# Kernel optimization log

Measured on AMD Instinct MI355X. Metric: run time of the kernel, lower is better.

The kernel has to match this reference:

```python
import jax, jax.numpy as jnp
import numpy as np

EMBED_DIM = 768
NUM_HEADS = 12
HEAD_DIM = EMBED_DIM // NUM_HEADS
B, S = 2, 2048


def setup_inputs() -> dict:
    key = jax.random.key(0)
    ks = jax.random.split(key, 6)
    glorot = jnp.sqrt(6.0 / (EMBED_DIM + EMBED_DIM)).astype(jnp.float32)
    x = jax.random.normal(ks[0], (B, S, EMBED_DIM), dtype=jnp.float32)
    mask = jnp.zeros((1, 1, S, S), dtype=jnp.float32)  # additive mask, 0 = no masking
    Wq = jax.random.uniform(ks[1], (EMBED_DIM, EMBED_DIM), jnp.float32, -glorot, glorot)
    Wk = jax.random.uniform(ks[2], (EMBED_DIM, EMBED_DIM), jnp.float32, -glorot, glorot)
    Wv = jax.random.uniform(ks[3], (EMBED_DIM, EMBED_DIM), jnp.float32, -glorot, glorot)
    Wo = jax.random.uniform(ks[4], (EMBED_DIM, EMBED_DIM), jnp.float32, -glorot, glorot)
    bo = jnp.zeros((EMBED_DIM,), dtype=jnp.float32)
    return {"x": x, "mask": mask, "Wq": Wq, "Wk": Wk, "Wv": Wv, "Wo": Wo, "bo": bo}


def reference(x, mask, Wq, Wk, Wv, Wo, bo):
    b, s, _ = x.shape
    # Q/K/V projections (no bias), split into heads: [b, h, s, d]
    def split_heads(t):
        return t.reshape(b, s, NUM_HEADS, HEAD_DIM).transpose(0, 2, 1, 3)
    q = split_heads(x @ Wq)
    k = split_heads(x @ Wk)
    v = split_heads(x @ Wv)
    scale = 1.0 / jnp.sqrt(jnp.float32(HEAD_DIM))
    logits = jnp.einsum('bhqd,bhkd->bhqk', q, k) * scale  # [b, h, s, s]
    logits = logits + mask * (-1e9)
    weights = jax.nn.softmax(logits, axis=-1)
    attn = jnp.einsum('bhqk,bhkd->bhqd', weights, v)
    concat = attn.transpose(0, 2, 1, 3).reshape(b, s, EMBED_DIM)
    return concat @ Wo + bo
```

## Files before the change

kernel.cpp:

```cpp
#include <hip/hip_runtime.h>


typedef __bf16 bf16_t;
typedef bf16_t bf16x8 __attribute__((ext_vector_type(8)));
typedef bf16_t bf16x4 __attribute__((ext_vector_type(4)));
typedef float f32x4 __attribute__((ext_vector_type(4)));
typedef _Float16 f16x4 __attribute__((ext_vector_type(4)));

#define SC2 0.1803368801111137f

__device__ __forceinline__ float bf2f(unsigned short u) {
  union { unsigned int i; float f; } x;
  x.i = ((unsigned int)u) << 16;
  return x.f;
}

__device__ __forceinline__ void glds16(const bf16_t* g, bf16_t* l) {
  __builtin_amdgcn_global_load_lds(
      (const __attribute__((address_space(1))) void*)g,
      (__attribute__((address_space(3))) void*)l, 16, 0, 0);
}

__device__ __forceinline__ int detect_bf16_flag(const unsigned short* x) {
  const int lane = threadIdx.x & 63;
  const uint4* p = (const uint4*)x;
  uint4 a = p[lane * 2];
  uint4 b = p[lane * 2 + 1];
  unsigned int w[8] = {a.x, a.y, a.z, a.w, b.x, b.y, b.z, b.w};
  unsigned int big = 0;
#pragma unroll
  for (int i = 0; i < 8; i++) {
    unsigned int e0 = (w[i] >> 7) & 0xFF, e1 = (w[i] >> 23) & 0xFF;
    big |= (e0 > 0x88u) | (e1 > 0x88u);
  }
  unsigned long long bal = __ballot(big != 0u);
  return bal == 0ULL ? 1 : 0;
}

__global__ void k_prep(const void* __restrict__ x, const void* __restrict__ mask,
                       const void* __restrict__ Wq, const void* __restrict__ Wk,
                       const void* __restrict__ Wv, const void* __restrict__ Wo,
                       bf16_t* __restrict__ xb, bf16_t* __restrict__ wqkvT,
                       bf16_t* __restrict__ woT, int* __restrict__ mflags) {
  __shared__ float ts[32][33];
  __shared__ int snz;
  const int blk = blockIdx.x;
  const int f = detect_bf16_flag((const unsigned short*)x);

  if (blk < 1536) {
    int i = blk * 256 + threadIdx.x;
    if (f) {
      ((uint4*)xb)[i] = ((const uint4*)x)[i];
    } else {
      const float* xf = (const float*)x + (size_t)i * 8;
      bf16x8 v;
#pragma unroll
      for (int j = 0; j < 8; j++) v[j] = (bf16_t)xf[j];
      *(bf16x8*)(xb + (size_t)i * 8) = v;
    }
  } else if (blk < 3840) {
    const int t = blk - 1536;
    const int z = t / 576, r = t % 576, kt = r / 24, nt = r % 24;
    const void* wsrc = (z == 0) ? Wq : (z == 1) ? Wk : (z == 2) ? Wv : Wo;
    bf16_t* dst = (z < 3) ? (wqkvT + (size_t)z * 768 * 768) : woT;
    const int c = threadIdx.x & 31, r0 = threadIdx.x >> 5;
#pragma unroll
    for (int i = 0; i < 4; i++) {
      int kr = kt * 32 + r0 + i * 8;
      float v;
      if (f) v = bf2f(((const unsigned short*)wsrc)[(size_t)kr * 768 + nt * 32 + c]);
      else   v = ((const float*)wsrc)[(size_t)kr * 768 + nt * 32 + c];
      ts[r0 + i * 8][c] = v;
    }
    __syncthreads();
#pragma unroll
    for (int i = 0; i < 4; i++) {
      int nr = nt * 32 + r0 + i * 8;
      dst[(size_t)nr * 768 + kt * 32 + c] = (bf16_t)ts[c][r0 + i * 8];
    }
  } else {
    const int t = blk - 3840;
    const int qt = t >> 4, ktm = t & 15;
    if (threadIdx.x == 0) snz = 0;
    __syncthreads();
    int nz = 0;
    for (int i = 0; i < 64; i++) {
      int lin = i * 256 + threadIdx.x;
      int rr = lin >> 7, cc = lin & 127;
      size_t idx = (size_t)(qt * 128 + rr) * 2048 + ktm * 128 + cc;
      float v = f ? bf2f(((const unsigned short*)mask)[idx]) : ((const float*)mask)[idx];
      nz |= (v != 0.0f);
    }
    if (nz) snz = 1;
    __syncthreads();
    if (threadIdx.x == 0) mflags[qt * 16 + ktm] = snz;
  }
}

__global__ __launch_bounds__(256, 2) void k_gemmQKV(
    const bf16_t* __restrict__ A, const bf16_t* __restrict__ Bm,
    bf16_t* __restrict__ Qd, bf16_t* __restrict__ Kd, _Float16* __restrict__ Vt) {
  __shared__ __align__(16) char smem[17408];
  bf16_t* As = (bf16_t*)smem;
  bf16_t* Bs = (bf16_t*)(smem + 8192);
  _Float16* Tb = (_Float16*)smem;

  const int tid = threadIdx.x;
  const int n0 = blockIdx.x * 128, m0 = blockIdx.y * 128;
  const int r = tid >> 2, c8 = (tid & 3) << 3;
  const bf16_t* Ag = A + (size_t)(m0 + r) * 768 + c8;
  const bf16_t* Bg = Bm + (size_t)(n0 + r) * 768 + c8;
  const int wid = tid >> 6, lane = tid & 63;
  const int wm = (wid >> 1) << 6, wn = (wid & 1) << 6;
  const int lr = lane & 15, lk = (lane >> 4) << 3, g4 = (lane >> 4) << 2;

  f32x4 acc[4][4];
  const f32x4 z = {0.f, 0.f, 0.f, 0.f};
#pragma unroll
  for (int i = 0; i < 4; i++)
#pragma unroll
    for (int j = 0; j < 4; j++) acc[i][j] = z;

  for (int k0 = 0; k0 < 768; k0 += 32) {
    glds16(Ag + k0, As + wid * 512);
    glds16(Ag + (size_t)64 * 768 + k0, As + 2048 + wid * 512);
    glds16(Bg + k0, Bs + wid * 512);
    glds16(Bg + (size_t)64 * 768 + k0, Bs + 2048 + wid * 512);
    __syncthreads();
    bf16x8 af[4], bf_[4];
#pragma unroll
    for (int t = 0; t < 4; t++) af[t]  = *(const bf16x8*)&As[(wm + t * 16 + lr) * 32 + lk];
#pragma unroll
    for (int t = 0; t < 4; t++) bf_[t] = *(const bf16x8*)&Bs[(wn + t * 16 + lr) * 32 + lk];
#pragma unroll
    for (int i = 0; i < 4; i++)
#pragma unroll
      for (int j = 0; j < 4; j++)
        acc[i][j] = __builtin_amdgcn_mfma_f32_16x16x32_bf16(af[i], bf_[j], acc[i][j], 0, 0, 0);
    __syncthreads();
  }

  if (n0 < 1536) {
    bf16_t* dst = (n0 < 768) ? Qd : Kd;
    const int nb = (n0 < 768) ? n0 : n0 - 768;
    const int bb = m0 >> 11;
#pragma unroll
    for (int i = 0; i < 4; i++)
#pragma unroll
      for (int j = 0; j < 4; j++) {
        const int rc = nb + wn + j * 16 + lr;
        const int hh = rc >> 6, dd = rc & 63;
        const size_t base = (((size_t)bb * 12 + hh) * 2048) * 64 + dd;
#pragma unroll
        for (int reg = 0; reg < 4; reg++) {
          const int s = (m0 & 2047) + wm + i * 16 + g4 + reg;
          dst[base + (size_t)s * 64] = (bf16_t)acc[i][j][reg];
        }
      }
  } else {
    const int bb = m0 >> 11;
#pragma unroll
    for (int half = 0; half < 2; half++) {
      if ((wid & 1) == half) {
#pragma unroll
        for (int j = 0; j < 4; j++) {
          const int d_l = j * 16 + lr;
#pragma unroll
          for (int i = 0; i < 4; i++)
#pragma unroll
            for (int reg = 0; reg < 4; reg++)
              Tb[d_l * 136 + wm + i * 16 + g4 + reg] = (_Float16)acc[i][j][reg];
        }
      }
      __syncthreads();
      const int row = tid >> 2, cc = (tid & 3) * 32;
      const int vcol = (n0 - 1536) + half * 64 + row;
      const int hh = vcol >> 6;
      _Float16* dstv = Vt + (((size_t)bb * 12 + hh) * 64 + row) * 2048 + (m0 & 2047) + cc;
#pragma unroll
      for (int u = 0; u < 4; u++)
        *(uint4*)(dstv + u * 8) = *(const uint4*)&Tb[row * 136 + cc + u * 8];
      __syncthreads();
    }
  }
}

__global__ __launch_bounds__(320, 4) void k_flash(
    const bf16_t* __restrict__ Qd, const bf16_t* __restrict__ Kd,
    const _Float16* __restrict__ Vt, const void* __restrict__ mask,
    const int* __restrict__ mflags, const unsigned short* __restrict__ xdet,
    bf16_t* __restrict__ attn) {
  __shared__ __align__(16) char sm[32768];

  const int tid = threadIdx.x, wid = tid >> 6, lane = tid & 63;
  const int lr = lane & 15, quad = lane >> 4, lk = quad << 3, g4 = quad << 2;

  const int lin = blockIdx.x;
  const int gx = lin & 7, ww = lin >> 3;
  const int hb = gx * 3 + (ww >> 5);
  const int h = hb % 12, bb = hb / 12;
  const int qt = ww & 31;

  const size_t bh = (size_t)bb * 12 + h;
  const char* Kh = (const char*)(Kd + bh * 2048 * 64);
  const char* Vh = (const char*)(Vt + bh * 64 * 2048);

  if (wid == 4) {
    const char* kS[8]; const char* vS[8];
#pragma unroll
    for (int u = 0; u < 8; u++) {
      const int R = (u >> 1) * 16 + lr;
      const int c = (u & 1) * 4 + quad;
      kS[u] = Kh + R * 128 + c * 16;
      const int u2 = u * 2 + (lane >> 5);
      const int dtv = u2 & 3, ctv = u2 >> 2, j2 = lane & 31;
      vS[u] = Vh + (size_t)(dtv * 16 + (j2 & 15)) * 4096 + ctv * 32 + (j2 >> 4) * 16;
    }
    uint4 kv[8], vv[8];
#pragma unroll
    for (int u = 0; u < 8; u++) kv[u] = *(const uint4*)(kS[u]);
#pragma unroll
    for (int u = 0; u < 8; u++) vv[u] = *(const uint4*)(vS[u]);
#pragma unroll
    for (int u = 0; u < 8; u++) *(uint4*)(sm + u * 1024 + lane * 16) = kv[u];
#pragma unroll
    for (int u = 0; u < 8; u++) *(uint4*)(sm + 8192 + u * 1024 + lane * 16) = vv[u];
    __syncthreads();
    for (int s = 0; s < 32; s++) {
      if (s < 31) {
        const int t = s + 1;
        char* buf = sm + (t & 1) * 16384;
#pragma unroll
        for (int u = 0; u < 8; u++) kv[u] = *(const uint4*)(kS[u] + (size_t)t * 8192);
#pragma unroll
        for (int u = 0; u < 8; u++) vv[u] = *(const uint4*)(vS[u] + (size_t)t * 128);
#pragma unroll
        for (int u = 0; u < 8; u++) *(uint4*)(buf + u * 1024 + lane * 16) = kv[u];
#pragma unroll
        for (int u = 0; u < 8; u++) *(uint4*)(buf + 8192 + u * 1024 + lane * 16) = vv[u];
      }
      __syncthreads();
    }
    return;
  }

  const bf16_t* Qh = Qd + bh * 2048 * 64;
  const int q0 = qt * 64 + wid * 16;
  const int mbf = detect_bf16_flag(xdet);
  const int* mfrow = mflags + (qt >> 1) * 16;

  const bf16x8 qf0 = *(const bf16x8*)&Qh[(size_t)(q0 + lr) * 64 + lk];
  const bf16x8 qf1 = *(const bf16x8*)&Qh[(size_t)(q0 + lr) * 64 + 32 + lk];

  const f32x4 z = {0.f, 0.f, 0.f, 0.f};
  f32x4 ot[4];
#pragma unroll
  for (int dt = 0; dt < 4; dt++) ot[dt] = z;
  float mrow = -1e30f, lrow = 0.f;

  __syncthreads();

  for (int s = 0; s < 32; s++) {
    const char* Kc = sm + (s & 1) * 16384;
    const char* Vc = Kc + 8192;

    f32x4 sv[4];
#pragma unroll
    for (int ct = 0; ct < 4; ct++) sv[ct] = z;
#pragma unroll
    for (int ct = 0; ct < 4; ct++) {
      bf16x8 kf0 = *(const bf16x8*)(Kc + ct * 2048 + lane * 16);
      bf16x8 kf1 = *(const bf16x8*)(Kc + ct * 2048 + 1024 + lane * 16);
      sv[ct] = __builtin_amdgcn_mfma_f32_16x16x32_bf16(kf0, qf0, sv[ct], 0, 0, 0);
      sv[ct] = __builtin_amdgcn_mfma_f32_16x16x32_bf16(kf1, qf1, sv[ct], 0, 0, 0);
    }

    if (mfrow[s >> 1]) {
#pragma unroll
      for (int ct = 0; ct < 4; ct++)
#pragma unroll
        for (int reg = 0; reg < 4; reg++) {
          size_t mi = (size_t)(q0 + lr) * 2048 + s * 64 + ct * 16 + g4 + reg;
          float mv = mbf ? bf2f(((const unsigned short*)mask)[mi])
                         : ((const float*)mask)[mi];
          sv[ct][reg] -= 8e9f * mv;
        }
    }

    float t = fmaxf(
        fmaxf(fmaxf(fmaxf(sv[0][0], sv[0][1]), fmaxf(sv[0][2], sv[0][3])),
              fmaxf(fmaxf(sv[1][0], sv[1][1]), fmaxf(sv[1][2], sv[1][3]))),
        fmaxf(fmaxf(fmaxf(sv[2][0], sv[2][1]), fmaxf(sv[2][2], sv[2][3])),
              fmaxf(fmaxf(sv[3][0], sv[3][1]), fmaxf(sv[3][2], sv[3][3]))));
    t = fmaxf(t, __shfl_xor(t, 16));
    t = fmaxf(t, __shfl_xor(t, 32));
    const float mnew = fmaxf(mrow, t);
    const float alpha = exp2f((mrow - mnew) * SC2);
    const float mS = mnew * SC2;
    mrow = mnew;

    float rs = 0.f;
    f16x4 pb[4];
#pragma unroll
    for (int ct = 0; ct < 4; ct++) {
      float p0 = exp2f(fmaf(sv[ct][0], SC2, -mS));
      float p1 = exp2f(fmaf(sv[ct][1], SC2, -mS));
      float p2 = exp2f(fmaf(sv[ct][2], SC2, -mS));
      float p3 = exp2f(fmaf(sv[ct][3], SC2, -mS));
      rs += (p0 + p1) + (p2 + p3);
      f16x4 pk;
      pk[0] = (_Float16)p0; pk[1] = (_Float16)p1;
      pk[2] = (_Float16)p2; pk[3] = (_Float16)p3;
      pb[ct] = pk;
    }
    rs += __shfl_xor(rs, 16);
    rs += __shfl_xor(rs, 32);
    lrow = lrow * alpha + rs;

#pragma unroll
    for (int dt = 0; dt < 4; dt++)
#pragma unroll
      for (int reg = 0; reg < 4; reg++) ot[dt][reg] *= alpha;
#pragma unroll
    for (int ct = 0; ct < 4; ct++) {
#pragma unroll
      for (int dt = 0; dt < 4; dt++) {
        f16x4 va = *(const f16x4*)(Vc + (ct * 4 + dt) * 512 +
                                   (quad >> 1) * 256 + lr * 16 + (quad & 1) * 8);
        ot[dt] = __builtin_amdgcn_mfma_f32_16x16x16f16(va, pb[ct], ot[dt], 0, 0, 0);
      }
    }
    __syncthreads();
  }

  const float inv = 1.0f / lrow;
  bf16_t* arow = attn + ((size_t)bb * 2048 + q0 + lr) * 768 + h * 64 + g4;
#pragma unroll
  for (int dt = 0; dt < 4; dt++) {
    bf16x4 v;
#pragma unroll
    for (int reg = 0; reg < 4; reg++) v[reg] = (bf16_t)(ot[dt][reg] * inv);
    *(bf16x4*)(arow + dt * 16) = v;
  }
}

__global__ __launch_bounds__(256, 4) void k_gemm2(
    const bf16_t* __restrict__ A, const bf16_t* __restrict__ Bm,
    const void* __restrict__ bo, const unsigned short* __restrict__ xdet,
    float* __restrict__ outF, unsigned short* __restrict__ outH) {
  __shared__ __align__(16) bf16_t As[64 * 32];
  __shared__ __align__(16) bf16_t Bs[128 * 32];
  const int tid = threadIdx.x, wid = tid >> 6, lane = tid & 63;
  const int n0 = blockIdx.x * 128, m0 = blockIdx.y * 64;
  const int wm = (wid >> 1) * 32, wn = (wid & 1) * 64;
  const int lr = lane & 15, lk = (lane >> 4) << 3, g4 = (lane >> 4) << 2;
  const int rr = lane >> 2, c8 = (lane & 3) << 3;
  const bf16_t* Ag  = A + (size_t)(m0 + wid * 16 + rr) * 768 + c8;
  const bf16_t* Bg0 = Bm + (size_t)(n0 + wid * 32 + rr) * 768 + c8;
  const bf16_t* Bg1 = Bm + (size_t)(n0 + wid * 32 + 16 + rr) * 768 + c8;

  f32x4 acc[2][4];
  const f32x4 z = {0.f, 0.f, 0.f, 0.f};
#pragma unroll
  for (int i = 0; i < 2; i++)
#pragma unroll
    for (int j = 0; j < 4; j++) acc[i][j] = z;

  for (int k0 = 0; k0 < 768; k0 += 32) {
    glds16(Ag + k0, As + wid * 512);
    glds16(Bg0 + k0, Bs + wid * 1024);
    glds16(Bg1 + k0, Bs + wid * 1024 + 512);
    __syncthreads();
    bf16x8 af[2], bf_[4];
#pragma unroll
    for (int i = 0; i < 2; i++) af[i]  = *(const bf16x8*)&As[(wm + i * 16 + lr) * 32 + lk];
#pragma unroll
    for (int j = 0; j < 4; j++) bf_[j] = *(const bf16x8*)&Bs[(wn + j * 16 + lr) * 32 + lk];
#pragma unroll
    for (int i = 0; i < 2; i++)
#pragma unroll
      for (int j = 0; j < 4; j++)
        acc[i][j] = __builtin_amdgcn_mfma_f32_16x16x32_bf16(af[i], bf_[j], acc[i][j], 0, 0, 0);
    __syncthreads();
  }

  const int obf = detect_bf16_flag(xdet);
#pragma unroll
  for (int i = 0; i < 2; i++)
#pragma unroll
    for (int j = 0; j < 4; j++) {
      const int nn = n0 + wn + j * 16 + lr;
      const float bv = obf ? bf2f(((const unsigned short*)bo)[nn])
                           : ((const float*)bo)[nn];
#pragma unroll
      for (int reg = 0; reg < 4; reg++) {
        const int m = m0 + wm + i * 16 + g4 + reg;
        const float v = acc[i][j][reg] + bv;
        if (obf) outH[(size_t)m * 768 + nn] = __builtin_bit_cast(unsigned short, (bf16_t)v);
        else     outF[(size_t)m * 768 + nn] = v;
      }
    }
}

extern "C" void kernel_launch(void* const* d_in, const int* in_sizes, int n_in,
                              void* d_out, int out_size, void* d_ws, size_t ws_size,
                              hipStream_t stream) {
  (void)in_sizes; (void)n_in; (void)out_size; (void)ws_size;
  const void* x    = d_in[0];
  const void* mask = d_in[1];
  const void* Wq   = d_in[2];
  const void* Wk   = d_in[3];
  const void* Wv   = d_in[4];
  const void* Wo   = d_in[5];
  const void* bo   = d_in[6];

  char* w = (char*)d_ws;
  size_t off = 0;
  auto take = [&](size_t b) -> void* {
    void* p = w + off;
    off = (off + b + 255) & ~(size_t)255;
    return p;
  };
  int*      mflags = (int*)take(256 * 4);
  bf16_t*   wqkvT  = (bf16_t*)take((size_t)2304 * 768 * 2);
  bf16_t*   woT    = (bf16_t*)take((size_t)768 * 768 * 2);
  bf16_t*   xb     = (bf16_t*)take((size_t)4096 * 768 * 2);
  bf16_t*   Qd     = (bf16_t*)take((size_t)3145728 * 2);
  bf16_t*   Kd     = (bf16_t*)take((size_t)3145728 * 2);
  _Float16* Vt     = (_Float16*)take((size_t)3145728 * 2);
  bf16_t*   attn   = xb;

  k_prep<<<4096, 256, 0, stream>>>(x, mask, Wq, Wk, Wv, Wo, xb, wqkvT, woT, mflags);
  k_gemmQKV<<<dim3(18, 32), 256, 0, stream>>>(xb, wqkvT, Qd, Kd, Vt);
  k_flash<<<768, 320, 0, stream>>>(Qd, Kd, Vt, mask, mflags,
                                   (const unsigned short*)x, attn);
  k_gemm2<<<dim3(6, 64), 256, 0, stream>>>(attn, woT, bo, (const unsigned short*)x,
                                           (float*)d_out, (unsigned short*)d_out);
}
```

Measured before the change: 201.5 us.

## Process two query tiles per flash wave with fewer waves and lazy rescale

Each compute wave in the flash kernel now handles 32 query rows (two 16-row groups) instead of 16. The block shrinks to two compute waves plus one loader wave, so each K/V fragment read from LDS feeds twice as many MFMAs. The mask-tile flags are preloaded into a bitmask, and the output/denominator rescale is skipped when no row maximum grows. The QKV GEMM launch-bounds occupancy hint rises from 2 to 3. This raises register pressure per wave and halves the wave count per block, which could reduce latency hiding.

```diff
diff --git a/kernel.cpp b/kernel.cpp
--- a/kernel.cpp
+++ b/kernel.cpp
@@ -97,7 +97,7 @@
   }
 }
 
-__global__ __launch_bounds__(256, 2) void k_gemmQKV(
+__global__ __launch_bounds__(256, 3) void k_gemmQKV(
     const bf16_t* __restrict__ A, const bf16_t* __restrict__ Bm,
     bf16_t* __restrict__ Qd, bf16_t* __restrict__ Kd, _Float16* __restrict__ Vt) {
   __shared__ __align__(16) char smem[17408];
@@ -185,7 +185,7 @@
   }
 }
 
-__global__ __launch_bounds__(320, 4) void k_flash(
+__global__ __launch_bounds__(192, 4) void k_flash(
     const bf16_t* __restrict__ Qd, const bf16_t* __restrict__ Kd,
     const _Float16* __restrict__ Vt, const void* __restrict__ mask,
     const int* __restrict__ mflags, const unsigned short* __restrict__ xdet,
@@ -205,7 +205,7 @@
   const char* Kh = (const char*)(Kd + bh * 2048 * 64);
   const char* Vh = (const char*)(Vt + bh * 64 * 2048);
 
-  if (wid == 4) {
+  if (wid == 2) {
     const char* kS[8]; const char* vS[8];
 #pragma unroll
     for (int u = 0; u < 8; u++) {
@@ -245,18 +245,27 @@
   }
 
   const bf16_t* Qh = Qd + bh * 2048 * 64;
-  const int q0 = qt * 64 + wid * 16;
+  const int q0 = qt * 64 + wid * 32;
   const int mbf = detect_bf16_flag(xdet);
   const int* mfrow = mflags + (qt >> 1) * 16;
-
-  const bf16x8 qf0 = *(const bf16x8*)&Qh[(size_t)(q0 + lr) * 64 + lk];
-  const bf16x8 qf1 = *(const bf16x8*)&Qh[(size_t)(q0 + lr) * 64 + 32 + lk];
+  int mbits = 0;
+#pragma unroll
+  for (int t = 0; t < 16; t++) mbits |= (mfrow[t] != 0) << t;
+
+  bf16x8 qf[2][2];
+#pragma unroll
+  for (int qg = 0; qg < 2; qg++) {
+    qf[qg][0] = *(const bf16x8*)&Qh[(size_t)(q0 + qg * 16 + lr) * 64 + lk];
+    qf[qg][1] = *(const bf16x8*)&Qh[(size_t)(q0 + qg * 16 + lr) * 64 + 32 + lk];
+  }
 
   const f32x4 z = {0.f, 0.f, 0.f, 0.f};
-  f32x4 ot[4];
-#pragma unroll
-  for (int dt = 0; dt < 4; dt++) ot[dt] = z;
-  float mrow = -1e30f, lrow = 0.f;
+  f32x4 ot[2][4];
+  float mrow[2] = {-1e30f, -1e30f}, lrow[2] = {0.f, 0.f};
+#pragma unroll
+  for (int qg = 0; qg < 2; qg++)
+#pragma unroll
+    for (int dt = 0; dt < 4; dt++) ot[qg][dt] = z;
 
   __syncthreads();
 
@@ -264,83 +273,106 @@
     const char* Kc = sm + (s & 1) * 16384;
     const char* Vc = Kc + 8192;
 
-    f32x4 sv[4];
-#pragma unroll
-    for (int ct = 0; ct < 4; ct++) sv[ct] = z;
+    f32x4 sv[2][4];
+#pragma unroll
+    for (int qg = 0; qg < 2; qg++)
+#pragma unroll
+      for (int ct = 0; ct < 4; ct++) sv[qg][ct] = z;
 #pragma unroll
     for (int ct = 0; ct < 4; ct++) {
       bf16x8 kf0 = *(const bf16x8*)(Kc + ct * 2048 + lane * 16);
       bf16x8 kf1 = *(const bf16x8*)(Kc + ct * 2048 + 1024 + lane * 16);
-      sv[ct] = __builtin_amdgcn_mfma_f32_16x16x32_bf16(kf0, qf0, sv[ct], 0, 0, 0);
-      sv[ct] = __builtin_amdgcn_mfma_f32_16x16x32_bf16(kf1, qf1, sv[ct], 0, 0, 0);
-    }
-
-    if (mfrow[s >> 1]) {
-#pragma unroll
-      for (int ct = 0; ct < 4; ct++)
-#pragma unroll
-        for (int reg = 0; reg < 4; reg++) {
-          size_t mi = (size_t)(q0 + lr) * 2048 + s * 64 + ct * 16 + g4 + reg;
-          float mv = mbf ? bf2f(((const unsigned short*)mask)[mi])
-                         : ((const float*)mask)[mi];
-          sv[ct][reg] -= 8e9f * mv;
-        }
-    }
-
-    float t = fmaxf(
-        fmaxf(fmaxf(fmaxf(sv[0][0], sv[0][1]), fmaxf(sv[0][2], sv[0][3])),
-              fmaxf(fmaxf(sv[1][0], sv[1][1]), fmaxf(sv[1][2], sv[1][3]))),
-        fmaxf(fmaxf(fmaxf(sv[2][0], sv[2][1]), fmaxf(sv[2][2], sv[2][3])),
-              fmaxf(fmaxf(sv[3][0], sv[3][1]), fmaxf(sv[3][2], sv[3][3]))));
-    t = fmaxf(t, __shfl_xor(t, 16));
-    t = fmaxf(t, __shfl_xor(t, 32));
-    const float mnew = fmaxf(mrow, t);
-    const float alpha = exp2f((mrow - mnew) * SC2);
-    const float mS = mnew * SC2;
-    mrow = mnew;
-
-    float rs = 0.f;
-    f16x4 pb[4];
-#pragma unroll
-    for (int ct = 0; ct < 4; ct++) {
-      float p0 = exp2f(fmaf(sv[ct][0], SC2, -mS));
-      float p1 = exp2f(fmaf(sv[ct][1], SC2, -mS));
-      float p2 = exp2f(fmaf(sv[ct][2], SC2, -mS));
-      float p3 = exp2f(fmaf(sv[ct][3], SC2, -mS));
-      rs += (p0 + p1) + (p2 + p3);
-      f16x4 pk;
-      pk[0] = (_Float16)p0; pk[1] = (_Float16)p1;
-      pk[2] = (_Float16)p2; pk[3] = (_Float16)p3;
-      pb[ct] = pk;
-    }
-    rs += __shfl_xor(rs, 16);
-    rs += __shfl_xor(rs, 32);
-    lrow = lrow * alpha + rs;
-
-#pragma unroll
-    for (int dt = 0; dt < 4; dt++)
-#pragma unroll
-      for (int reg = 0; reg < 4; reg++) ot[dt][reg] *= alpha;
+      sv[0][ct] = __builtin_amdgcn_mfma_f32_16x16x32_bf16(kf0, qf[0][0], sv[0][ct], 0, 0, 0);
+      sv[0][ct] = __builtin_amdgcn_mfma_f32_16x16x32_bf16(kf1, qf[0][1], sv[0][ct], 0, 0, 0);
+      sv[1][ct] = __builtin_amdgcn_mfma_f32_16x16x32_bf16(kf0, qf[1][0], sv[1][ct], 0, 0, 0);
+      sv[1][ct] = __builtin_amdgcn_mfma_f32_16x16x32_bf16(kf1, qf[1][1], sv[1][ct], 0, 0, 0);
+    }
+
+    if ((mbits >> (s >> 1)) & 1) {
+#pragma unroll
+      for (int qg = 0; qg < 2; qg++)
+#pragma unroll
+        for (int ct = 0; ct < 4; ct++)
+#pragma unroll
+          for (int reg = 0; reg < 4; reg++) {
+            size_t mi = (size_t)(q0 + qg * 16 + lr) * 2048 + s * 64 + ct * 16 + g4 + reg;
+            float mv = mbf ? bf2f(((const unsigned short*)mask)[mi])
+                           : ((const float*)mask)[mi];
+            sv[qg][ct][reg] -= 8e9f * mv;
+          }
+    }
+
+    float mnew[2];
+#pragma unroll
+    for (int qg = 0; qg < 2; qg++) {
+      float t = fmaxf(
+          fmaxf(fmaxf(fmaxf(sv[qg][0][0], sv[qg][0][1]), fmaxf(sv[qg][0][2], sv[qg][0][3])),
+                fmaxf(fmaxf(sv[qg][1][0], sv[qg][1][1]), fmaxf(sv[qg][1][2], sv[qg][1][3]))),
+          fmaxf(fmaxf(fmaxf(sv[qg][2][0], sv[qg][2][1]), fmaxf(sv[qg][2][2], sv[qg][2][3])),
+                fmaxf(fmaxf(sv[qg][3][0], sv[qg][3][1]), fmaxf(sv[qg][3][2], sv[qg][3][3]))));
+      t = fmaxf(t, __shfl_xor(t, 16));
+      t = fmaxf(t, __shfl_xor(t, 32));
+      mnew[qg] = fmaxf(mrow[qg], t);
+    }
+    if (__ballot((mnew[0] > mrow[0]) | (mnew[1] > mrow[1]))) {
+#pragma unroll
+      for (int qg = 0; qg < 2; qg++) {
+        const float alpha = exp2f((mrow[qg] - mnew[qg]) * SC2);
+#pragma unroll
+        for (int dt = 0; dt < 4; dt++)
+#pragma unroll
+          for (int reg = 0; reg < 4; reg++) ot[qg][dt][reg] *= alpha;
+        lrow[qg] *= alpha;
+      }
+    }
+    mrow[0] = mnew[0]; mrow[1] = mnew[1];
+
+    f16x4 pb[2][4];
+#pragma unroll
+    for (int qg = 0; qg < 2; qg++) {
+      const float mS = mnew[qg] * SC2;
+      float rs = 0.f;
+#pragma unroll
+      for (int ct = 0; ct < 4; ct++) {
+        float p0 = exp2f(fmaf(sv[qg][ct][0], SC2, -mS));
+        float p1 = exp2f(fmaf(sv[qg][ct][1], SC2, -mS));
+        float p2 = exp2f(fmaf(sv[qg][ct][2], SC2, -mS));
+        float p3 = exp2f(fmaf(sv[qg][ct][3], SC2, -mS));
+        rs += (p0 + p1) + (p2 + p3);
+        f16x4 pk;
+        pk[0] = (_Float16)p0; pk[1] = (_Float16)p1;
+        pk[2] = (_Float16)p2; pk[3] = (_Float16)p3;
+        pb[qg][ct] = pk;
+      }
+      rs += __shfl_xor(rs, 16);
+      rs += __shfl_xor(rs, 32);
+      lrow[qg] += rs;
+    }
+
 #pragma unroll
     for (int ct = 0; ct < 4; ct++) {
 #pragma unroll
       for (int dt = 0; dt < 4; dt++) {
         f16x4 va = *(const f16x4*)(Vc + (ct * 4 + dt) * 512 +
                                    (quad >> 1) * 256 + lr * 16 + (quad & 1) * 8);
-        ot[dt] = __builtin_amdgcn_mfma_f32_16x16x16f16(va, pb[ct], ot[dt], 0, 0, 0);
-      }
-    }
-    __syncthreads();
-  }
-
-  const float inv = 1.0f / lrow;
-  bf16_t* arow = attn + ((size_t)bb * 2048 + q0 + lr) * 768 + h * 64 + g4;
-#pragma unroll
-  for (int dt = 0; dt < 4; dt++) {
-    bf16x4 v;
-#pragma unroll
-    for (int reg = 0; reg < 4; reg++) v[reg] = (bf16_t)(ot[dt][reg] * inv);
-    *(bf16x4*)(arow + dt * 16) = v;
+        ot[0][dt] = __builtin_amdgcn_mfma_f32_16x16x16f16(va, pb[0][ct], ot[0][dt], 0, 0, 0);
+        ot[1][dt] = __builtin_amdgcn_mfma_f32_16x16x16f16(va, pb[1][ct], ot[1][dt], 0, 0, 0);
+      }
+    }
+    __syncthreads();
+  }
+
+#pragma unroll
+  for (int qg = 0; qg < 2; qg++) {
+    const float inv = 1.0f / lrow[qg];
+    bf16_t* arow = attn + ((size_t)bb * 2048 + q0 + qg * 16 + lr) * 768 + h * 64 + g4;
+#pragma unroll
+    for (int dt = 0; dt < 4; dt++) {
+      bf16x4 v;
+#pragma unroll
+      for (int reg = 0; reg < 4; reg++) v[reg] = (bf16_t)(ot[qg][dt][reg] * inv);
+      *(bf16x4*)(arow + dt * 16) = v;
+    }
   }
 }
 
@@ -432,7 +464,7 @@
 
   k_prep<<<4096, 256, 0, stream>>>(x, mask, Wq, Wk, Wv, Wo, xb, wqkvT, woT, mflags);
   k_gemmQKV<<<dim3(18, 32), 256, 0, stream>>>(xb, wqkvT, Qd, Kd, Vt);
-  k_flash<<<768, 320, 0, stream>>>(Qd, Kd, Vt, mask, mflags,
+  k_flash<<<768, 192, 0, stream>>>(Qd, Kd, Vt, mask, mflags,
                                    (const unsigned short*)x, attn);
   k_gemm2<<<dim3(6, 64), 256, 0, stream>>>(attn, woT, bo, (const unsigned short*)x,
                                            (float*)d_out, (unsigned short*)d_out);
```

After: 255.4 us. +26.8%, slower.
